# Kernel optimization log

Hardware: AMD Instinct MI355X
Metric: run time of the kernel (lower is better)

The kernel has to match this reference:

```python
import jax, jax.numpy as jnp
import numpy as np

LAMDA = 0.5  # weight between agent-selected hidden state and current hidden state
SAMPLE_SEED = 42  # RNG for categorical action sampling (torch version is stochastic)


def setup_inputs() -> dict:
    B, T, D, H, U, A = 256, 512, 128, 128, 64, 10
    key = jax.random.key(0)
    ks = jax.random.split(key, 16)
    s = 0.1
    return {
        "x": jax.random.normal(ks[0], (B, T, D), dtype=jnp.float32),
        "mask": jnp.ones((B, T), dtype=jnp.int32),
        # GRUCell params (torch layout: [3H, in], gate order r,z,n)
        "gru_w_ih": jax.random.normal(ks[1], (3 * H, D), dtype=jnp.float32) * s,
        "gru_w_hh": jax.random.normal(ks[2], (3 * H, H), dtype=jnp.float32) * s,
        "gru_b_ih": jnp.zeros((3 * H,), dtype=jnp.float32),
        "gru_b_hh": jnp.zeros((3 * H,), dtype=jnp.float32),
        # agent1 MLP: observes mean of hidden buffer ([B,H])
        "a1_w1": jax.random.normal(ks[3], (U, H), dtype=jnp.float32) * s,
        "a1_b1": jnp.zeros((U,), dtype=jnp.float32),
        "a1_w2": jax.random.normal(ks[4], (A, U), dtype=jnp.float32) * s,
        "a1_b2": jnp.zeros((A,), dtype=jnp.float32),
        # agent2 MLP: observes current input ([B,D])
        "a2_w1": jax.random.normal(ks[5], (U, D), dtype=jnp.float32) * s,
        "a2_b1": jnp.zeros((U,), dtype=jnp.float32),
        "a2_w2": jax.random.normal(ks[6], (A, U), dtype=jnp.float32) * s,
        "a2_b2": jnp.zeros((A,), dtype=jnp.float32),
    }


def _gru_cell(xt, h, w_ih, w_hh, b_ih, b_hh):
    gi = xt @ w_ih.T + b_ih  # [B, 3H]
    gh = h @ w_hh.T + b_hh
    ir, iz, inn = jnp.split(gi, 3, axis=-1)
    hr, hz, hn = jnp.split(gh, 3, axis=-1)
    r = jax.nn.sigmoid(ir + hr)
    z = jax.nn.sigmoid(iz + hz)
    n = jnp.tanh(inn + r * hn)
    return (1.0 - z) * n + z * h


def _agent_action(obs, w1, b1, w2, b2, key):
    # observation is detached in the original (choose_action detaches)
    z = jnp.tanh(jax.lax.stop_gradient(obs) @ w1.T + b1)
    logits = z @ w2.T + b2  # Categorical(softmax(logits)) == categorical over logits
    return jax.random.categorical(key, logits, axis=-1)  # [B]


def reference(x, mask, gru_w_ih, gru_w_hh, gru_b_ih, gru_b_hh,
              a1_w1, a1_b1, a1_w2, a1_b2, a2_w1, a2_b1, a2_w2, a2_b2):
    B, T, D = x.shape
    H = gru_w_hh.shape[1]
    A = a1_w2.shape[0]
    keys = jax.random.split(jax.random.key(SAMPLE_SEED), 2 * T).reshape(T, 2)

    gru = lambda xt, h: _gru_cell(xt, h, gru_w_ih, gru_w_hh, gru_b_ih, gru_b_hh)

    # t == 0: cur_h is zeros, action_h == cur_h, so weighted_h == 0; agent samples
    # at t=0 are discarded for state (they only fill RL bookkeeping lists).
    h0 = gru(x[:, 0], jnp.zeros((B, H), x.dtype))
    buf0 = jnp.zeros((A, B, H), x.dtype)  # observed_h history buffer
    bidx = jnp.arange(B)

    def step(carry, inp):
        h, buf = carry
        xt, kt = inp
        buf = jnp.concatenate([buf[1:], h[None]], axis=0)  # shift in previous hidden
        a1 = _agent_action(buf.mean(axis=0), a1_w1, a1_b1, a1_w2, a1_b2, kt[0])
        a2 = _agent_action(xt, a2_w1, a2_b1, a2_w2, a2_b2, kt[1])
        action_h = (buf[a1, bidx] + buf[a2, bidx]) * 0.5  # [B,H] gather of past states
        weighted_h = LAMDA * action_h + (1.0 - LAMDA) * h
        hn = gru(xt, weighted_h)
        return (hn, buf), hn

    xs = (jnp.swapaxes(x[:, 1:], 0, 1), keys[1:])  # time-major
    _, hs = jax.lax.scan(step, (h0, buf0), xs)
    h_all = jnp.swapaxes(jnp.concatenate([h0[None], hs], axis=0), 0, 1)  # [B,T,H]

    last_idx = jnp.sum(mask, axis=1) - 1  # get_last_visit
    last_out = h_all[bidx, last_idx]  # [B,H]; dropout=0.0 -> identity
    return last_out, h_all
```

## Files before the change

kernel.cpp:

```cpp
#include <hip/hip_runtime.h>
#include <math.h>

#define B_ 256
#define T_ 512
#define D_ 128
#define H_ 128
#define BH_ 32768
#define NG 1308160

__device__ __forceinline__ void bar_lds() {
  asm volatile("s_waitcnt lgkmcnt(0)\n\ts_barrier" ::: "memory");
}

__device__ __forceinline__ float dpp_add_xor1(float v) {
  int r = __builtin_amdgcn_update_dpp(0, __float_as_int(v), 0xB1, 0xF, 0xF, true);
  return v + __int_as_float(r);
}
__device__ __forceinline__ float dpp_add_xor2(float v) {
  int r = __builtin_amdgcn_update_dpp(0, __float_as_int(v), 0x4E, 0xF, 0xF, true);
  return v + __int_as_float(r);
}

__device__ __forceinline__ float frcp(float x) { return __builtin_amdgcn_rcpf(x); }
__device__ __forceinline__ float fsigmoid(float x) { return frcp(1.0f + __expf(-x)); }
__device__ __forceinline__ float ftanh_(float x) { return 1.0f - 2.0f * frcp(1.0f + __expf(2.0f * x)); }

__device__ __forceinline__ void tf2x32(unsigned k0, unsigned k1, unsigned x0, unsigned x1,
                                       unsigned& o0, unsigned& o1) {
  unsigned k2 = k0 ^ k1 ^ 0x1BD11BDAu;
  unsigned v0 = x0 + k0, v1 = x1 + k1;
#define TFR(r) { v0 += v1; v1 = (v1 << (r)) | (v1 >> (32 - (r))); v1 ^= v0; }
  TFR(13) TFR(15) TFR(26) TFR(6)   v0 += k1; v1 += k2 + 1u;
  TFR(17) TFR(29) TFR(16) TFR(24)  v0 += k2; v1 += k0 + 2u;
  TFR(13) TFR(15) TFR(26) TFR(6)   v0 += k0; v1 += k1 + 3u;
  TFR(17) TFR(29) TFR(16) TFR(24)  v0 += k1; v1 += k2 + 4u;
  TFR(13) TFR(15) TFR(26) TFR(6)   v0 += k2; v1 += k0 + 5u;
#undef TFR
  o0 = v0; o1 = v1;
}

__device__ __forceinline__ float gumbel_f(unsigned bits) {
  const float tiny = 1.17549435e-38f;
  float u = __uint_as_float((bits >> 9) | 0x3f800000u) - 1.0f;
  u = u + tiny;
  u = fmaxf(tiny, u);
  return -__logf(-__logf(u));
}

__global__ void p0_keys(unsigned* __restrict__ keys_tab) {
  int i = blockIdx.x * blockDim.x + threadIdx.x;
  if (i >= 1024) return;
  unsigned o0, o1;
  tf2x32(0u, 42u, 0u, (unsigned)i, o0, o1);
  keys_tab[2 * i] = o0; keys_tab[2 * i + 1] = o1;
}

#define SX 264
#define SW 72
__global__ __launch_bounds__(256, 4) void gemm_tiled(
    const float* __restrict__ x, const float* __restrict__ w_ih,
    const float* __restrict__ b_ih, const float* __restrict__ a2w1,
    const float* __restrict__ a2b1, float* __restrict__ gi, float* __restrict__ zt) {
  __shared__ __align__(16) float Xs[32 * SX];
  __shared__ __align__(16) float Ws[32 * SW];
  const int tid = threadIdx.x;
  const int mb = blockIdx.x & 511;
  const int nb = blockIdx.x >> 9;
  const bool isz = (nb == 6);
  const size_t m0 = (size_t)mb * 256;
  const int n0 = isz ? 0 : nb * 64;
  const float* wsrc = isz ? a2w1 : w_ih;
  const float* bsrc = isz ? a2b1 : b_ih;
  const int mt = tid >> 4;
  const int nt = tid & 15;
  const int kg = tid >> 5;
  const int ri = tid & 31;

  float acc[16][4];
  #pragma unroll
  for (int i = 0; i < 16; i++)
    #pragma unroll
    for (int j = 0; j < 4; j++) acc[i][j] = 0.f;

  #pragma unroll 1
  for (int kc = 0; kc < 4; kc++) {
    const int k0 = kc * 32;
    __syncthreads();
    #pragma unroll
    for (int p = 0; p < 8; p++) {
      int row = ri + 32 * p;
      float4 v = *(const float4*)(x + (m0 + row) * 128 + k0 + 4 * kg);
      Xs[(4 * kg + 0) * SX + row] = v.x;
      Xs[(4 * kg + 1) * SX + row] = v.y;
      Xs[(4 * kg + 2) * SX + row] = v.z;
      Xs[(4 * kg + 3) * SX + row] = v.w;
    }
    #pragma unroll
    for (int p = 0; p < 2; p++) {
      int n = ri + 32 * p;
      float4 v = *(const float4*)(wsrc + (size_t)(n0 + n) * 128 + k0 + 4 * kg);
      Ws[(4 * kg + 0) * SW + n] = v.x;
      Ws[(4 * kg + 1) * SW + n] = v.y;
      Ws[(4 * kg + 2) * SW + n] = v.z;
      Ws[(4 * kg + 3) * SW + n] = v.w;
    }
    __syncthreads();
    #pragma unroll 4
    for (int kk = 0; kk < 32; kk++) {
      const float* xrow = Xs + kk * SX + mt * 16;
      float4 xa0 = ((const float4*)xrow)[0];
      float4 xa1 = ((const float4*)xrow)[1];
      float4 xa2 = ((const float4*)xrow)[2];
      float4 xa3 = ((const float4*)xrow)[3];
      float4 wv = *(const float4*)(Ws + kk * SW + nt * 4);
      float xv[16] = {xa0.x, xa0.y, xa0.z, xa0.w, xa1.x, xa1.y, xa1.z, xa1.w,
                      xa2.x, xa2.y, xa2.z, xa2.w, xa3.x, xa3.y, xa3.z, xa3.w};
      #pragma unroll
      for (int i = 0; i < 16; i++) {
        acc[i][0] += xv[i] * wv.x;
        acc[i][1] += xv[i] * wv.y;
        acc[i][2] += xv[i] * wv.z;
        acc[i][3] += xv[i] * wv.w;
      }
    }
  }
  float4 bias = *(const float4*)(bsrc + n0 + nt * 4);
  if (!isz) {
    #pragma unroll
    for (int i = 0; i < 16; i++) {
      float4 o;
      o.x = acc[i][0] + bias.x; o.y = acc[i][1] + bias.y;
      o.z = acc[i][2] + bias.z; o.w = acc[i][3] + bias.w;
      size_t m = m0 + (size_t)mt * 16 + i;
      *(float4*)(gi + m * 384 + n0 + nt * 4) = o;
    }
  } else {
    #pragma unroll
    for (int i = 0; i < 16; i++) {
      float4 o;
      o.x = ftanh_(acc[i][0] + bias.x); o.y = ftanh_(acc[i][1] + bias.y);
      o.z = ftanh_(acc[i][2] + bias.z); o.w = ftanh_(acc[i][3] + bias.w);
      size_t m = m0 + (size_t)mt * 16 + i;
      *(float4*)(zt + m * 64 + nt * 4) = o;
    }
  }
}

__global__ __launch_bounds__(256) void sampler(
    const float* __restrict__ zt, const float* __restrict__ w2,
    const float* __restrict__ b2, const unsigned* __restrict__ keys_tab,
    float* __restrict__ g1, int* __restrict__ a2_tab) {
  __shared__ __align__(16) float w2s[10][68];
  __shared__ float b2s[10];
  __shared__ __align__(16) float zs[4][64];
  const int tid = threadIdx.x, w = tid >> 6, lane = tid & 63;
  const int t = blockIdx.x + 1;
  for (int i = tid; i < 640; i += 256) w2s[i >> 6][i & 63] = w2[i];
  if (tid < 10) b2s[tid] = b2[tid];
  __syncthreads();
  const unsigned k0a = keys_tab[2 * (2 * t + 1)], k1a = keys_tab[2 * (2 * t + 1) + 1];
  const unsigned k0g = keys_tab[2 * (2 * t)],     k1g = keys_tab[2 * (2 * t) + 1];
  const int a = lane & 15, kc = lane >> 4;
  float zr = zt[((size_t)w * 512 + t) * 64 + lane];
  #pragma unroll 1
  for (int it = 0; it < 64; it++) {
    const int b = 4 * it + w;
    zs[w][lane] = zr;
    if (it < 63) zr = zt[((size_t)(b + 4) * 512 + t) * 64 + lane];
    float p = 0.f;
    if (a < 10) {
      const float4* zp = (const float4*)(&zs[w][16 * kc]);
      const float4* wp = (const float4*)(&w2s[a][16 * kc]);
      #pragma unroll
      for (int c = 0; c < 4; c++) {
        float4 zv = zp[c], w4 = wp[c];
        p += w4.x * zv.x + w4.y * zv.y + w4.z * zv.z + w4.w * zv.w;
      }
    }
    p += __shfl_xor(p, 16);
    p += __shfl_xor(p, 32);
    float val = -3.0e38f;
    if (a < 10 && kc == 0) {
      unsigned o0, o1;
      tf2x32(k0a, k1a, 0u, (unsigned)(b * 10 + a), o0, o1);
      val = (p + b2s[a]) + gumbel_f(o0 ^ o1);
      tf2x32(k0g, k1g, 0u, (unsigned)(b * 10 + a), o0, o1);
      g1[((size_t)(t - 1) * 256 + b) * 10 + a] = gumbel_f(o0 ^ o1);
    }
    float best = 0.f; int bi = 0;
    #pragma unroll
    for (int aa = 0; aa < 10; aa++) {
      float v = __shfl(val, aa);
      if (aa == 0 || v > best) { best = v; bi = aa; }
    }
    if (lane == 0) a2_tab[(size_t)(t - 1) * 256 + b] = bi;
  }
}

__global__ __launch_bounds__(512, 1) void seq_kernel(
    const float* __restrict__ gi_glob, const int* __restrict__ mask,
    const float* __restrict__ w_hh, const float* __restrict__ b_hh,
    const float* __restrict__ a1w1, const float* __restrict__ a1b1,
    const float* __restrict__ a1w2, const float* __restrict__ a1b2,
    const float* __restrict__ g1_tab, const int* __restrict__ a2_tab,
    float* __restrict__ out) {
  __shared__ __align__(16) float ring2[20][128];
  __shared__ __align__(16) float slotrec[10][512];
  __shared__ __align__(16) float ghi4[512];
  __shared__ __align__(16) float hbuf[128];
  __shared__ __align__(16) float obs[128];
  __shared__ __align__(16) float osum[128];
  __shared__ __align__(16) float z1buf[64];
  __shared__ __align__(16) float lastbuf[128];
  __shared__ __align__(16) float w2buf[10][68];
  __shared__ float b1s[64], b2s[10];
  __shared__ float g1buf[10];
  __shared__ float2 pl2[16];
  __shared__ int a2s_lds;
  __shared__ int redi[8];
  __shared__ int last_s;

  const int tid = threadIdx.x;
  const int wave = tid >> 6, lane = tid & 63;
  const int b = blockIdx.x;

  float4 wr[4][8];
  const int q = tid >> 2, qk = tid & 3;
  if (tid < 384) {
    #pragma unroll
    for (int i = 0; i < 4; i++) {
      const float* basep = w_hh + (size_t)(4 * q + i) * 128 + 4 * qk;
      #pragma unroll
      for (int c = 0; c < 8; c++) wr[i][c] = *(const float4*)(basep + 16 * c);
    }
  }
  float4 w1reg[16];
  if (wave >= 6) {
    int m = ((wave - 6) << 5) + (lane >> 1);
    int kc = lane & 1;
    const float4* wp = (const float4*)(a1w1 + (size_t)m * 128 + 64 * kc);
    #pragma unroll
    for (int c = 0; c < 16; c++) w1reg[c] = wp[c];
  }
  float bhh6[6] = {0.f, 0.f, 0.f, 0.f, 0.f, 0.f};
  float gc[6] = {0.f, 0.f, 0.f, 0.f, 0.f, 0.f};
  if (wave == 6) {
    bhh6[0] = b_hh[lane];       bhh6[1] = b_hh[128 + lane]; bhh6[2] = b_hh[256 + lane];
    bhh6[3] = b_hh[64 + lane];  bhh6[4] = b_hh[192 + lane]; bhh6[5] = b_hh[320 + lane];
    const float* p1 = gi_glob + ((size_t)b * 512 + 1) * 384;
    gc[0] = p1[lane];      gc[1] = p1[128 + lane]; gc[2] = p1[256 + lane];
    gc[3] = p1[64 + lane]; gc[4] = p1[192 + lane]; gc[5] = p1[320 + lane];
  }
  float g1r = 0.f; int a2r = 0;
  if (wave == 7 && lane < 10) g1r = g1_tab[(size_t)b * 10 + lane];
  if (wave == 7 && lane == 12) a2r = a2_tab[b];

  for (int idx = tid; idx < 2560; idx += 512) ((float*)ring2)[idx] = 0.f;
  for (int idx = tid; idx < 5120; idx += 512) ((float*)slotrec)[idx] = 0.f;
  for (int idx = tid; idx < 640; idx += 512) w2buf[idx >> 6][idx & 63] = a1w2[idx];
  if (tid < 64) b1s[tid] = a1b1[tid];
  if (tid < 10) b2s[tid] = a1b2[tid];
  int mv = mask[(size_t)b * T_ + tid];
  #pragma unroll
  for (int off = 1; off < 64; off <<= 1) mv += __shfl_xor(mv, off);
  if (lane == 0) redi[wave] = mv;
  __syncthreads();
  if (tid == 0) {
    int s = 0;
    #pragma unroll
    for (int w = 0; w < 8; w++) s += redi[w];
    last_s = s - 1;
  }
  __syncthreads();
  const int last = last_s;

  if (tid < 128) {
    int j = tid;
    const float* g0 = gi_glob + (size_t)b * 512 * 384;
    float r  = fsigmoid(g0[j] + b_hh[j]);
    float zz = fsigmoid(g0[128 + j] + b_hh[128 + j]);
    float n  = ftanh_(g0[256 + j] + r * b_hh[256 + j]);
    float hnew = (1.0f - zz) * n;
    hbuf[j] = hnew; ring2[0][j] = hnew; ring2[10][j] = hnew;
    slotrec[0][(j << 2) + 3] = hnew;
    obs[j] = hnew / 10.0f;
    __builtin_nontemporal_store(hnew, &out[BH_ + ((size_t)b * 512) * 128 + j]);
    if (0 == last) lastbuf[j] = hnew;
  }
  __syncthreads();

  #pragma unroll 1
  for (int t = 1; t < T_; t++) {
    const int sn = (t + 9) % 10;
    if (tid < 384) {
      const float4* hb4 = (const float4*)hbuf;
      float4 a0 = make_float4(0.f, 0.f, 0.f, 0.f), a1v = a0, a2v = a0, a3v = a0;
      #pragma unroll
      for (int c = 0; c < 8; c++) {
        float4 h4 = hb4[4 * c + qk];
        a0.x += wr[0][c].x * h4.x; a0.y += wr[0][c].y * h4.y; a0.z += wr[0][c].z * h4.z; a0.w += wr[0][c].w * h4.w;
        a1v.x += wr[1][c].x * h4.x; a1v.y += wr[1][c].y * h4.y; a1v.z += wr[1][c].z * h4.z; a1v.w += wr[1][c].w * h4.w;
        a2v.x += wr[2][c].x * h4.x; a2v.y += wr[2][c].y * h4.y; a2v.z += wr[2][c].z * h4.z; a2v.w += wr[2][c].w * h4.w;
        a3v.x += wr[3][c].x * h4.x; a3v.y += wr[3][c].y * h4.y; a3v.z += wr[3][c].z * h4.z; a3v.w += wr[3][c].w * h4.w;
      }
      float s0  = (a0.x + a0.y) + (a0.z + a0.w);
      float s1v = (a1v.x + a1v.y) + (a1v.z + a1v.w);
      float s2v = (a2v.x + a2v.y) + (a2v.z + a2v.w);
      float s3v = (a3v.x + a3v.y) + (a3v.z + a3v.w);
      s0  = dpp_add_xor2(dpp_add_xor1(s0));
      s1v = dpp_add_xor2(dpp_add_xor1(s1v));
      s2v = dpp_add_xor2(dpp_add_xor1(s2v));
      s3v = dpp_add_xor2(dpp_add_xor1(s3v));
      float my = (qk == 0) ? s0 : (qk == 1) ? s1v : (qk == 2) ? s2v : s3v;
      slotrec[sn][((tid & 127) << 2) + (tid >> 7)] = my;
      if (tid >= 128 && tid < 256) {
        int j = tid - 128;
        int bs = (t + 1) % 10;
        float s = 0.f;
        #pragma unroll
        for (int a = 0; a < 9; a++) s += ring2[bs + a][j];
        osum[j] = s;
      }
    } else if (wave == 6) {
      __builtin_amdgcn_s_setprio(1);
      float4 e0, e1;
      e0.x = gc[0] + bhh6[0]; e0.y = gc[1] + bhh6[1]; e0.z = gc[2]; e0.w = bhh6[2];
      e1.x = gc[3] + bhh6[3]; e1.y = gc[4] + bhh6[4]; e1.z = gc[5]; e1.w = bhh6[5];
      ((float4*)ghi4)[lane] = e0;
      ((float4*)ghi4)[64 + lane] = e1;
      float gn0 = 0.f, gn1 = 0.f, gn2 = 0.f, gn3 = 0.f, gn4 = 0.f, gn5 = 0.f;
      if (t < 511) {
        const float* bp = gi_glob + ((size_t)b * 512 + t + 1) * 384;
        gn0 = bp[lane];      gn1 = bp[128 + lane]; gn2 = bp[256 + lane];
        gn3 = bp[64 + lane]; gn4 = bp[192 + lane]; gn5 = bp[320 + lane];
      }
      {
        int m = lane >> 1, kc = lane & 1;
        float ax = 0.f, ay = 0.f, az = 0.f, aw = 0.f;
        #pragma unroll
        for (int c = 0; c < 16; c++) {
          float4 o4 = ((const float4*)obs)[16 * kc + c];
          ax += w1reg[c].x * o4.x; ay += w1reg[c].y * o4.y;
          az += w1reg[c].z * o4.z; aw += w1reg[c].w * o4.w;
        }
        float d = (ax + ay) + (az + aw);
        d = dpp_add_xor1(d);
        if (kc == 0) z1buf[m] = ftanh_(d + b1s[m]);
      }
      if (lane < 40) {
        int a = lane >> 2, k2 = lane & 3;
        int m0 = 8 * k2;
        float4 z4a = ((const float4*)(z1buf + m0))[0], z4b = ((const float4*)(z1buf + m0))[1];
        float4 wa = ((const float4*)(&w2buf[a][m0]))[0], wb = ((const float4*)(&w2buf[a][m0]))[1];
        float p = z4a.x * wa.x + z4a.y * wa.y + z4a.z * wa.z + z4a.w * wa.w
                + z4b.x * wb.x + z4b.y * wb.y + z4b.z * wb.z + z4b.w * wb.w;
        p = dpp_add_xor2(dpp_add_xor1(p));
        if (k2 == 0) pl2[a].x = p + b2s[a];
      }
      gc[0] = gn0; gc[1] = gn1; gc[2] = gn2; gc[3] = gn3; gc[4] = gn4; gc[5] = gn5;
      __builtin_amdgcn_s_setprio(0);
    } else {
      __builtin_amdgcn_s_setprio(1);
      if (lane < 10) g1buf[lane] = g1r;
      if (lane == 12) a2s_lds = a2r;
      if (t < 511) {
        if (lane < 10) g1r = g1_tab[((size_t)t * 256 + b) * 10 + lane];
        if (lane == 12) a2r = a2_tab[(size_t)t * 256 + b];
      }
      {
        int m = 32 + (lane >> 1), kc = lane & 1;
        float ax = 0.f, ay = 0.f, az = 0.f, aw = 0.f;
        #pragma unroll
        for (int c = 0; c < 16; c++) {
          float4 o4 = ((const float4*)obs)[16 * kc + c];
          ax += w1reg[c].x * o4.x; ay += w1reg[c].y * o4.y;
          az += w1reg[c].z * o4.z; aw += w1reg[c].w * o4.w;
        }
        float d = (ax + ay) + (az + aw);
        d = dpp_add_xor1(d);
        if (kc == 0) z1buf[m] = ftanh_(d + b1s[m]);
      }
      if (lane < 40) {
        int a = lane >> 2, k2 = lane & 3;
        int m0 = 32 + 8 * k2;
        float4 z4a = ((const float4*)(z1buf + m0))[0], z4b = ((const float4*)(z1buf + m0))[1];
        float4 wa = ((const float4*)(&w2buf[a][m0]))[0], wb = ((const float4*)(&w2buf[a][m0]))[1];
        float p = z4a.x * wa.x + z4a.y * wa.y + z4a.z * wa.z + z4a.w * wa.w
                + z4b.x * wb.x + z4b.y * wb.y + z4b.z * wb.z + z4b.w * wb.w;
        p = dpp_add_xor2(dpp_add_xor1(p));
        if (k2 == 0) pl2[a].y = p + g1buf[a];
      }
      __builtin_amdgcn_s_setprio(0);
    }
    bar_lds();

    if (tid < 128) {
      float best = 0.f; int bi = 0;
      #pragma unroll
      for (int a = 0; a < 10; a++) {
        float2 pv = pl2[a];
        float v = pv.x + pv.y;
        if (a == 0 || v > best) { best = v; bi = a; }
      }
      const int s1 = (t + bi) % 10;
      const int s2 = (t + a2s_lds) % 10;
      int j = tid;
      float4 y1 = *(const float4*)(&slotrec[s1][j << 2]);
      float4 y2 = *(const float4*)(&slotrec[s2][j << 2]);
      float4 yn = *(const float4*)(&slotrec[sn][j << 2]);
      float4 gv = ((const float4*)ghi4)[j];
      float gh1 = 0.5f * (0.5f * (y1.x + y2.x)) + 0.5f * yn.x;
      float gh2 = 0.5f * (0.5f * (y1.y + y2.y)) + 0.5f * yn.y;
      float gh3 = gv.w + 0.5f * (0.5f * (y1.z + y2.z)) + 0.5f * yn.z;
      float r  = fsigmoid(gv.x + gh1);
      float zz = fsigmoid(gv.y + gh2);
      float n  = ftanh_(gv.z + r * gh3);
      float hw = 0.5f * ((y1.w + y2.w) * 0.5f) + 0.5f * yn.w;
      float hnew = (1.0f - zz) * n + zz * hw;
      hbuf[j] = hnew;
      ring2[t % 10][j] = hnew;
      ring2[t % 10 + 10][j] = hnew;
      slotrec[t % 10][(j << 2) + 3] = hnew;
      __builtin_nontemporal_store(hnew, &out[BH_ + ((size_t)b * 512 + t) * 128 + j]);
      if (t == last) lastbuf[j] = hnew;
      obs[j] = (osum[j] + hnew) / 10.0f;
    }
    bar_lds();
  }
  if (tid < 128) __builtin_nontemporal_store(lastbuf[tid], &out[(size_t)b * H_ + tid]);
}

extern "C" void kernel_launch(void* const* d_in, const int* in_sizes, int n_in,
                              void* d_out, int out_size, void* d_ws, size_t ws_size,
                              hipStream_t stream) {
  (void)in_sizes; (void)n_in; (void)out_size; (void)ws_size;
  const float* x     = (const float*)d_in[0];
  const int*   mask  = (const int*)d_in[1];
  const float* w_ih  = (const float*)d_in[2];
  const float* w_hh  = (const float*)d_in[3];
  const float* b_ih  = (const float*)d_in[4];
  const float* b_hh  = (const float*)d_in[5];
  const float* a1w1  = (const float*)d_in[6];
  const float* a1b1  = (const float*)d_in[7];
  const float* a1w2  = (const float*)d_in[8];
  const float* a1b2  = (const float*)d_in[9];
  const float* a2w1  = (const float*)d_in[10];
  const float* a2b1  = (const float*)d_in[11];
  const float* a2w2  = (const float*)d_in[12];
  const float* a2b2  = (const float*)d_in[13];
  float* out = (float*)d_out;

  float*    gi       = (float*)d_ws;
  float*    g1       = gi + (size_t)131072 * 384;
  unsigned* keys_tab = (unsigned*)(g1 + NG);
  int*      a2_tab   = (int*)(keys_tab + 2048);
  float*    zt       = (float*)(a2_tab + 130816);

  p0_keys<<<4, 256, 0, stream>>>(keys_tab);
  gemm_tiled<<<3584, 256, 0, stream>>>(x, w_ih, b_ih, a2w1, a2b1, gi, zt);
  sampler<<<511, 256, 0, stream>>>(zt, a2w2, a2b2, keys_tab, g1, a2_tab);
  seq_kernel<<<256, 512, 0, stream>>>(gi, mask, w_hh, b_hh,
                                      a1w1, a1b1, a1w2, a1b2, g1, a2_tab, out);
}
```

Before: 1.048 ms.

## Double seq_kernel block to 1024 threads and halve matvec rows per thread

```diff
diff --git a/kernel.cpp b/kernel.cpp
--- a/kernel.cpp
+++ b/kernel.cpp
@@ -197,7 +197,7 @@
   }
 }
 
-__global__ __launch_bounds__(512, 1) void seq_kernel(
+__global__ __launch_bounds__(1024, 1) void seq_kernel(
     const float* __restrict__ gi_glob, const int* __restrict__ mask,
     const float* __restrict__ w_hh, const float* __restrict__ b_hh,
     const float* __restrict__ a1w1, const float* __restrict__ a1b1,
@@ -223,20 +223,20 @@
   const int tid = threadIdx.x;
   const int wave = tid >> 6, lane = tid & 63;
   const int b = blockIdx.x;
-
-  float4 wr[4][8];
-  const int q = tid >> 2, qk = tid & 3;
-  if (tid < 384) {
-    #pragma unroll
-    for (int i = 0; i < 4; i++) {
-      const float* basep = w_hh + (size_t)(4 * q + i) * 128 + 4 * qk;
+  const int qd = tid >> 2, qk = tid & 3;
+
+  float4 wq[2][8];
+  if (tid < 768) {
+    #pragma unroll
+    for (int r = 0; r < 2; r++) {
+      const float* basep = w_hh + (size_t)(2 * qd + r) * 128 + 4 * qk;
       #pragma unroll
-      for (int c = 0; c < 8; c++) wr[i][c] = *(const float4*)(basep + 16 * c);
+      for (int c = 0; c < 8; c++) wq[r][c] = *(const float4*)(basep + 16 * c);
     }
   }
   float4 w1reg[16];
-  if (wave >= 6) {
-    int m = ((wave - 6) << 5) + (lane >> 1);
+  if (wave == 12 || wave == 13) {
+    int m = ((wave - 12) << 5) + (lane >> 1);
     int kc = lane & 1;
     const float4* wp = (const float4*)(a1w1 + (size_t)m * 128 + 64 * kc);
     #pragma unroll
@@ -244,7 +244,7 @@
   }
   float bhh6[6] = {0.f, 0.f, 0.f, 0.f, 0.f, 0.f};
   float gc[6] = {0.f, 0.f, 0.f, 0.f, 0.f, 0.f};
-  if (wave == 6) {
+  if (wave == 12) {
     bhh6[0] = b_hh[lane];       bhh6[1] = b_hh[128 + lane]; bhh6[2] = b_hh[256 + lane];
     bhh6[3] = b_hh[64 + lane];  bhh6[4] = b_hh[192 + lane]; bhh6[5] = b_hh[320 + lane];
     const float* p1 = gi_glob + ((size_t)b * 512 + 1) * 384;
@@ -252,18 +252,20 @@
     gc[3] = p1[64 + lane]; gc[4] = p1[192 + lane]; gc[5] = p1[320 + lane];
   }
   float g1r = 0.f; int a2r = 0;
-  if (wave == 7 && lane < 10) g1r = g1_tab[(size_t)b * 10 + lane];
-  if (wave == 7 && lane == 12) a2r = a2_tab[b];
-
-  for (int idx = tid; idx < 2560; idx += 512) ((float*)ring2)[idx] = 0.f;
-  for (int idx = tid; idx < 5120; idx += 512) ((float*)slotrec)[idx] = 0.f;
-  for (int idx = tid; idx < 640; idx += 512) w2buf[idx >> 6][idx & 63] = a1w2[idx];
+  if (wave == 13 && lane < 10) g1r = g1_tab[(size_t)b * 10 + lane];
+  if (wave == 13 && lane == 12) a2r = a2_tab[b];
+
+  for (int idx = tid; idx < 2560; idx += 1024) ((float*)ring2)[idx] = 0.f;
+  for (int idx = tid; idx < 5120; idx += 1024) ((float*)slotrec)[idx] = 0.f;
+  if (tid < 640) w2buf[tid >> 6][tid & 63] = a1w2[tid];
   if (tid < 64) b1s[tid] = a1b1[tid];
   if (tid < 10) b2s[tid] = a1b2[tid];
-  int mv = mask[(size_t)b * T_ + tid];
-  #pragma unroll
-  for (int off = 1; off < 64; off <<= 1) mv += __shfl_xor(mv, off);
-  if (lane == 0) redi[wave] = mv;
+  if (tid < 512) {
+    int mv = mask[(size_t)b * T_ + tid];
+    #pragma unroll
+    for (int off = 1; off < 64; off <<= 1) mv += __shfl_xor(mv, off);
+    if (lane == 0) redi[wave] = mv;
+  }
   __syncthreads();
   if (tid == 0) {
     int s = 0;
@@ -292,27 +294,25 @@
   #pragma unroll 1
   for (int t = 1; t < T_; t++) {
     const int sn = (t + 9) % 10;
-    if (tid < 384) {
+    if (tid < 768) {
       const float4* hb4 = (const float4*)hbuf;
-      float4 a0 = make_float4(0.f, 0.f, 0.f, 0.f), a1v = a0, a2v = a0, a3v = a0;
+      float4 acc0 = make_float4(0.f, 0.f, 0.f, 0.f), acc1 = acc0;
       #pragma unroll
       for (int c = 0; c < 8; c++) {
         float4 h4 = hb4[4 * c + qk];
-        a0.x += wr[0][c].x * h4.x; a0.y += wr[0][c].y * h4.y; a0.z += wr[0][c].z * h4.z; a0.w += wr[0][c].w * h4.w;
-        a1v.x += wr[1][c].x * h4.x; a1v.y += wr[1][c].y * h4.y; a1v.z += wr[1][c].z * h4.z; a1v.w += wr[1][c].w * h4.w;
-        a2v.x += wr[2][c].x * h4.x; a2v.y += wr[2][c].y * h4.y; a2v.z += wr[2][c].z * h4.z; a2v.w += wr[2][c].w * h4.w;
-        a3v.x += wr[3][c].x * h4.x; a3v.y += wr[3][c].y * h4.y; a3v.z += wr[3][c].z * h4.z; a3v.w += wr[3][c].w * h4.w;
-      }
-      float s0  = (a0.x + a0.y) + (a0.z + a0.w);
-      float s1v = (a1v.x + a1v.y) + (a1v.z + a1v.w);
-      float s2v = (a2v.x + a2v.y) + (a2v.z + a2v.w);
-      float s3v = (a3v.x + a3v.y) + (a3v.z + a3v.w);
-      s0  = dpp_add_xor2(dpp_add_xor1(s0));
-      s1v = dpp_add_xor2(dpp_add_xor1(s1v));
-      s2v = dpp_add_xor2(dpp_add_xor1(s2v));
-      s3v = dpp_add_xor2(dpp_add_xor1(s3v));
-      float my = (qk == 0) ? s0 : (qk == 1) ? s1v : (qk == 2) ? s2v : s3v;
-      slotrec[sn][((tid & 127) << 2) + (tid >> 7)] = my;
+        acc0.x += wq[0][c].x * h4.x; acc0.y += wq[0][c].y * h4.y;
+        acc0.z += wq[0][c].z * h4.z; acc0.w += wq[0][c].w * h4.w;
+        acc1.x += wq[1][c].x * h4.x; acc1.y += wq[1][c].y * h4.y;
+        acc1.z += wq[1][c].z * h4.z; acc1.w += wq[1][c].w * h4.w;
+      }
+      float s0 = (acc0.x + acc0.y) + (acc0.z + acc0.w);
+      float s1 = (acc1.x + acc1.y) + (acc1.z + acc1.w);
+      s0 = dpp_add_xor2(dpp_add_xor1(s0));
+      s1 = dpp_add_xor2(dpp_add_xor1(s1));
+      if (qk < 2) {
+        int row = 2 * qd + qk;
+        slotrec[sn][((row & 127) << 2) + (row >> 7)] = qk ? s1 : s0;
+      }
       if (tid >= 128 && tid < 256) {
         int j = tid - 128;
         int bs = (t + 1) % 10;
@@ -321,8 +321,7 @@
         for (int a = 0; a < 9; a++) s += ring2[bs + a][j];
         osum[j] = s;
       }
-    } else if (wave == 6) {
-      __builtin_amdgcn_s_setprio(1);
+    } else if (wave == 12) {
       float4 e0, e1;
       e0.x = gc[0] + bhh6[0]; e0.y = gc[1] + bhh6[1]; e0.z = gc[2]; e0.w = bhh6[2];
       e1.x = gc[3] + bhh6[3]; e1.y = gc[4] + bhh6[4]; e1.z = gc[5]; e1.w = bhh6[5];
@@ -358,9 +357,7 @@
         if (k2 == 0) pl2[a].x = p + b2s[a];
       }
       gc[0] = gn0; gc[1] = gn1; gc[2] = gn2; gc[3] = gn3; gc[4] = gn4; gc[5] = gn5;
-      __builtin_amdgcn_s_setprio(0);
-    } else {
-      __builtin_amdgcn_s_setprio(1);
+    } else if (wave == 13) {
       if (lane < 10) g1buf[lane] = g1r;
       if (lane == 12) a2s_lds = a2r;
       if (t < 511) {
@@ -390,11 +387,11 @@
         p = dpp_add_xor2(dpp_add_xor1(p));
         if (k2 == 0) pl2[a].y = p + g1buf[a];
       }
-      __builtin_amdgcn_s_setprio(0);
     }
     bar_lds();
 
-    if (tid < 128) {
+    if (tid >= 896) {
+      const int j = tid & 127;
       float best = 0.f; int bi = 0;
       #pragma unroll
       for (int a = 0; a < 10; a++) {
@@ -404,7 +401,6 @@
       }
       const int s1 = (t + bi) % 10;
       const int s2 = (t + a2s_lds) % 10;
-      int j = tid;
       float4 y1 = *(const float4*)(&slotrec[s1][j << 2]);
       float4 y2 = *(const float4*)(&slotrec[s2][j << 2]);
       float4 yn = *(const float4*)(&slotrec[sn][j << 2]);
@@ -459,6 +455,6 @@
   p0_keys<<<4, 256, 0, stream>>>(keys_tab);
   gemm_tiled<<<3584, 256, 0, stream>>>(x, w_ih, b_ih, a2w1, a2b1, gi, zt);
   sampler<<<511, 256, 0, stream>>>(zt, a2w2, a2b2, keys_tab, g1, a2_tab);
-  seq_kernel<<<256, 512, 0, stream>>>(gi, mask, w_hh, b_hh,
-                                      a1w1, a1b1, a1w2, a1b2, g1, a2_tab, out);
-}
+  seq_kernel<<<256, 1024, 0, stream>>>(gi, mask, w_hh, b_hh,
+                                       a1w1, a1b1, a1w2, a1b2, g1, a2_tab, out);
+}
```

New measurement: 2.354 ms. 2.25x slower.
